# Performance work log

Measured on AMD Instinct MI355X. Metric: run time of the kernel, lower is better.

Reference implementation:

```python
import jax, jax.numpy as jnp
import numpy as np

B, L, T, V = 64, 512, 1000, 256
E, H, M, S = 256, 512, 80, 128  # text_embed, hidden, n_mels, speaker_dim


def lstm_scan(x, Wih, Whh, b):
    # x: [T, B, D]; torch gate order i, f, g, o; bias = b_ih + b_hh fused
    Bn = x.shape[1]
    Hn = Whh.shape[1]
    h0 = jnp.zeros((Bn, Hn), x.dtype)

    def step(carry, xt):
        h, c = carry
        g = xt @ Wih.T + h @ Whh.T + b
        i, f, gg, o = jnp.split(g, 4, axis=-1)
        c = jax.nn.sigmoid(f) * c + jax.nn.sigmoid(i) * jnp.tanh(gg)
        h = jax.nn.sigmoid(o) * jnp.tanh(c)
        return (h, c), h

    _, ys = jax.lax.scan(step, (h0, h0), x)
    return ys  # [T, B, H]


def setup_inputs() -> dict:
    key = jax.random.key(0)
    ks = jax.random.split(key, 32)
    r = lambda i, shp: (jax.random.normal(ks[i], shp, jnp.float32) * 0.1)
    Hd = H // 2  # 256, per-direction biLSTM hidden
    inp = {
        "text_input": jax.random.randint(ks[0], (B, L), 0, V),
        "speaker_embedding": jax.random.normal(ks[1], (B, S), jnp.float32),
        "target_mel": jax.random.normal(ks[2], (B, T, M), jnp.float32),
        "embed": r(3, (V, E)),
        # bidirectional text LSTM (hidden//2 per direction)
        "enc_Wih_f": r(4, (4 * Hd, E)), "enc_Whh_f": r(5, (4 * Hd, Hd)), "enc_b_f": r(6, (4 * Hd,)),
        "enc_Wih_b": r(7, (4 * Hd, E)), "enc_Whh_b": r(8, (4 * Hd, Hd)), "enc_b_b": r(9, (4 * Hd,)),
        # speaker projection MLP
        "sp_W1": r(10, (H, S)), "sp_b1": r(11, (H,)),
        "sp_W2": r(12, (H, H)), "sp_b2": r(13, (H,)),
        # 2-layer decoder LSTM, input = H + M = 592
        "dec_Wih0": r(14, (4 * H, H + M)), "dec_Whh0": r(15, (4 * H, H)), "dec_b0": r(16, (4 * H,)),
        "dec_Wih1": r(17, (4 * H, H)), "dec_Whh1": r(18, (4 * H, H)), "dec_b1": r(19, (4 * H,)),
        # mel projection MLP
        "mel_W1": r(20, (H, H)), "mel_b1": r(21, (H,)),
        "mel_W2": r(22, (M, H)), "mel_b2": r(23, (M,)),
        # stop token projection
        "stop_W": r(24, (1, H)), "stop_b": r(25, (1,)),
    }
    return inp


def reference(text_input, speaker_embedding, target_mel, embed,
              enc_Wih_f, enc_Whh_f, enc_b_f, enc_Wih_b, enc_Whh_b, enc_b_b,
              sp_W1, sp_b1, sp_W2, sp_b2,
              dec_Wih0, dec_Whh0, dec_b0, dec_Wih1, dec_Whh1, dec_b1,
              mel_W1, mel_b1, mel_W2, mel_b2, stop_W, stop_b):
    # --- text encoder: embedding + biLSTM ---
    x = jnp.swapaxes(embed[text_input], 0, 1)  # [L, B, E]
    fwd = lstm_scan(x, enc_Wih_f, enc_Whh_f, enc_b_f)          # [L, B, H/2]
    bwd = lstm_scan(x[::-1], enc_Wih_b, enc_Whh_b, enc_b_b)[::-1]
    text_encoded = jnp.swapaxes(jnp.concatenate([fwd, bwd], -1), 0, 1)  # [B, L, H]

    # --- speaker projection, broadcast over text length ---
    sp = jax.nn.relu(speaker_embedding @ sp_W1.T + sp_b1) @ sp_W2.T + sp_b2  # [B, H]
    encoder_output = text_encoded + sp[:, None, :]  # [B, L, H]

    # --- teacher-forced decoder: query_t = encoder_output[:, t % L] ---
    idx = jnp.arange(T) % L
    query = encoder_output[:, idx]  # [B, T, H]
    dec_mel_in = jnp.concatenate(
        [jnp.zeros((B, 1, M), target_mel.dtype), target_mel[:, :-1]], axis=1)  # [B, T, M]
    rnn_in = jnp.swapaxes(jnp.concatenate([dec_mel_in, query], -1), 0, 1)  # [T, B, H+M]

    h1 = lstm_scan(rnn_in, dec_Wih0, dec_Whh0, dec_b0)  # [T, B, H]
    h2 = lstm_scan(h1, dec_Wih1, dec_Whh1, dec_b1)      # [T, B, H]
    out = jnp.swapaxes(h2, 0, 1)  # [B, T, H]

    mel_outputs = jax.nn.relu(out @ mel_W1.T + mel_b1) @ mel_W2.T + mel_b2  # [B, T, M]
    stop_outputs = out @ stop_W.T + stop_b  # [B, T, 1]
    return mel_outputs, stop_outputs
```

## Files before the change

### kernel.cpp

```cpp
#include <hip/hip_runtime.h>
#include <cstdint>
#include <cstddef>


#define DEVI __device__ __forceinline__

typedef short bf16x8 __attribute__((ext_vector_type(8)));
typedef float f32x4 __attribute__((ext_vector_type(4)));
typedef unsigned short u16x4 __attribute__((ext_vector_type(4)));

constexpr int B_ = 64, L_ = 512, T_ = 1000, E_ = 256, H_ = 512, M_ = 80, S_ = 128, Hd_ = 256;

DEVI unsigned short f2bs(float f) {
  unsigned u = __builtin_bit_cast(unsigned, f);
  unsigned r = u + 0x7fffu + ((u >> 16) & 1u);
  return (unsigned short)(r >> 16);
}
DEVI float b2f(unsigned short s) { return __builtin_bit_cast(float, (unsigned)s << 16); }
DEVI void split2(float v, unsigned short& hi, unsigned short& lo) {
  hi = f2bs(v);
  lo = f2bs(v - b2f(hi));
}

DEVI float sigm(float x) { x = fminf(fmaxf(x, -30.f), 30.f); return 1.f / (1.f + __expf(-x)); }
DEVI float tanh_(float x) { x = fminf(fmaxf(x, -15.f), 15.f); float e = __expf(2.f * x); return (e - 1.f) / (e + 1.f); }

DEVI f32x4 mfma16(bf16x8 a, bf16x8 b, f32x4 c) {
  return __builtin_amdgcn_mfma_f32_16x16x32_bf16(a, b, c, 0, 0, 0);
}

DEVI void ld16c(bf16x8& r, const unsigned short* p) {
  asm volatile("global_load_dwordx4 %0, %1, off sc0 sc1" : "=v"(r) : "v"(p));
}
DEVI void st4c(unsigned short* p, unsigned v) {
  asm volatile("global_store_dword %0, %1, off sc0 sc1" :: "v"(p), "v"(v));
}
DEVI void st8c(unsigned short* p, u16x4 v) {
  asm volatile("global_store_dwordx2 %0, %1, off sc0 sc1" :: "v"(p), "v"(v));
}
#define VM_DRAIN() do { asm volatile("s_waitcnt vmcnt(0)" ::: "memory"); \
                        __builtin_amdgcn_sched_barrier(0); } while (0)
#define VM_WAIT8_OR_0(LAST) do { \
    if (LAST) asm volatile("s_waitcnt vmcnt(0)" ::: "memory"); \
    else      asm volatile("s_waitcnt vmcnt(8)" ::: "memory"); \
    __builtin_amdgcn_sched_barrier(0); } while (0)

struct Bar { int sub[8][64]; int master[64]; int release[64]; };

DEVI void grid_bar(Bar* bb, int nwg, int step) {
  __syncthreads();
  if (threadIdx.x == 0) {
    const int per = nwg >> 3;
    int old = __hip_atomic_fetch_add(&bb->sub[blockIdx.x & 7][0], 1, __ATOMIC_RELAXED, __HIP_MEMORY_SCOPE_AGENT);
    if (old == per * (step + 1) - 1) {
      int om = __hip_atomic_fetch_add(&bb->master[0], 1, __ATOMIC_RELAXED, __HIP_MEMORY_SCOPE_AGENT);
      if (om == 8 * (step + 1) - 1)
        __hip_atomic_fetch_add(&bb->release[0], 1, __ATOMIC_RELAXED, __HIP_MEMORY_SCOPE_AGENT);
    }
    while (__hip_atomic_fetch_add(&bb->release[0], 0, __ATOMIC_RELAXED, __HIP_MEMORY_SCOPE_AGENT) < step + 1)
      __builtin_amdgcn_s_sleep(2);
  }
  __syncthreads();
}

__global__ void k_prep(const float* __restrict__ embed, const float* __restrict__ tmel,
                       const float* __restrict__ mw1, const float* __restrict__ mw2,
                       unsigned short* emb_h, unsigned short* emb_l,
                       unsigned short* mel_h, unsigned short* mel_l,
                       unsigned short* w1_bf, unsigned short* w2_bf) {
  const long long stride = (long long)gridDim.x * blockDim.x;
  const long long i0 = (long long)blockIdx.x * blockDim.x + threadIdx.x;
  for (long long i = i0; i < 256 * 256; i += stride) {
    unsigned short h, l; split2(embed[i], h, l);
    emb_h[i] = h; emb_l[i] = l;
  }
  for (long long i = i0; i < (long long)T_ * B_ * 96; i += stride) {
    int c = (int)(i % 96);
    long long tb = i / 96;
    int b = (int)(tb % B_);
    int t = (int)(tb / B_);
    float v = 0.f;
    if (t > 0 && c < 80) v = tmel[((long long)b * T_ + (t - 1)) * M_ + c];
    unsigned short h, l; split2(v, h, l);
    mel_h[i] = h; mel_l[i] = l;
  }
  for (long long i = i0; i < 512 * 512; i += stride) w1_bf[i] = f2bs(mw1[i]);
  for (long long i = i0; i < 80 * 512; i += stride) w2_bf[i] = f2bs(mw2[i]);
}

__global__ void __launch_bounds__(512) k_sp(const float* __restrict__ spk,
                                            const float* __restrict__ w1, const float* __restrict__ b1,
                                            const float* __restrict__ w2, const float* __restrict__ b2,
                                            float* sp) {
  __shared__ float t1[512];
  const int b = blockIdx.x, j = threadIdx.x;
  float a = b1[j];
  const float* sr = spk + b * S_;
  for (int k = 0; k < S_; ++k) a += sr[k] * w1[j * S_ + k];
  t1[j] = fmaxf(a, 0.f);
  __syncthreads();
  float a2 = b2[j];
  for (int k = 0; k < H_; ++k) a2 += t1[k] * w2[j * H_ + k];
  sp[b * H_ + j] = a2;
}

constexpr int ENC_LDS = 2 * 16 * 4 * 64 * 16 + 4 * 64 * 16 * 4 + 256;

__global__ void __launch_bounds__(256) k_enc(
    const int* __restrict__ text,
    const float* __restrict__ WihF, const float* __restrict__ WhhF, const float* __restrict__ bF,
    const float* __restrict__ WihB, const float* __restrict__ WhhB, const float* __restrict__ bB,
    const unsigned short* __restrict__ emb_h, const unsigned short* __restrict__ emb_l,
    const float* __restrict__ sp,
    unsigned short* hench, unsigned short* hencl,
    unsigned short* ench, unsigned short* encl, Bar* bar) {
  extern __shared__ char lds[];
  unsigned short* Wh = (unsigned short*)lds;
  unsigned short* Wl = Wh + 16 * 4 * 64 * 8;
  float* G = (float*)(lds + 2 * 16 * 4 * 64 * 16);
  float* bias = G + 4 * 64 * 16;

  const int wg = blockIdx.x;
  const int dir = wg >> 4;
  const int jhb = (wg & 15) * 16;
  const int tid = threadIdx.x;
  const int wv = tid >> 6, ln = tid & 63, lg = ln >> 4, lr = ln & 15;

  const float* Wih = dir ? WihB : WihF;
  const float* Whh = dir ? WhhB : WhhF;
  const float* bb = dir ? bB : bF;

  for (int s = tid; s < 16 * 4 * 64; s += 256) {
    int kb = s >> 8, g = (s >> 6) & 3, l = s & 63;
    int R = g * Hd_ + jhb + (l & 15);
    int k0 = kb * 32 + (l >> 4) * 8;
    const float* src = (k0 < E_) ? (Wih + (size_t)R * E_ + k0) : (Whh + (size_t)R * Hd_ + (k0 - E_));
    bf16x8 vh, vl;
#pragma unroll
    for (int j = 0; j < 8; ++j) {
      unsigned short a, b; split2(src[j], a, b);
      vh[j] = (short)a; vl[j] = (short)b;
    }
    *(bf16x8*)(Wh + (size_t)s * 8) = vh;
    *(bf16x8*)(Wl + (size_t)s * 8) = vl;
  }
  if (tid < 64) bias[tid] = bb[(tid >> 4) * Hd_ + jhb + (tid & 15)];

  const int eb = tid >> 2, ej0 = (tid & 3) * 4;
  float c4[4] = {0.f, 0.f, 0.f, 0.f};
  float spv[4];
#pragma unroll
  for (int q = 0; q < 4; ++q) spv[q] = sp[eb * H_ + dir * Hd_ + jhb + ej0 + q];

  __syncthreads();

  for (int t = 0; t < L_; ++t) {
    const int tpos = dir ? (L_ - 1 - t) : t;
    const unsigned short* hsh = hench + (size_t)((t & 1) * 2 + dir) * B_ * Hd_;
    const unsigned short* hsl = hencl + (size_t)((t & 1) * 2 + dir) * B_ * Hd_;
    unsigned short* hdh = hench + (size_t)(((t + 1) & 1) * 2 + dir) * B_ * Hd_;
    unsigned short* hdl = hencl + (size_t)(((t + 1) & 1) * 2 + dir) * B_ * Hd_;

    for (int i = tid; i < 4096; i += 256) G[i] = bias[((i >> 10) << 4) + (i & 15)];

    int tix[4];
#pragma unroll
    for (int m = 0; m < 4; ++m) tix[m] = text[(16 * m + lr) * L_ + tpos];

    f32x4 acc[4][4];
#pragma unroll
    for (int g = 0; g < 4; ++g)
#pragma unroll
      for (int m = 0; m < 4; ++m) acc[g][m] = (f32x4){0.f, 0.f, 0.f, 0.f};

    auto MFE = [&](int kb, bf16x8 (&ah)[4], bf16x8 (&al)[4]) {
#pragma unroll
      for (int g = 0; g < 4; ++g) {
        bf16x8 bh = *(bf16x8*)(Wh + ((size_t)(kb * 4 + g) * 64 + ln) * 8);
        bf16x8 bl = *(bf16x8*)(Wl + ((size_t)(kb * 4 + g) * 64 + ln) * 8);
#pragma unroll
        for (int m = 0; m < 4; ++m) {
          acc[g][m] = mfma16(ah[m], bh, acc[g][m]);
          acc[g][m] = mfma16(al[m], bh, acc[g][m]);
          acc[g][m] = mfma16(ah[m], bl, acc[g][m]);
        }
      }
    };

    for (int kb = wv; kb < 8; kb += 4) {
      int k0 = kb * 32 + lg * 8;
      bf16x8 ah[4], al[4];
#pragma unroll
      for (int m = 0; m < 4; ++m) {
        ah[m] = *(const bf16x8*)(emb_h + (size_t)tix[m] * E_ + k0);
        al[m] = *(const bf16x8*)(emb_l + (size_t)tix[m] * E_ + k0);
      }
      MFE(kb, ah, al);
    }
    {
      auto issueE = [&](int kb, bf16x8 (&ah)[4], bf16x8 (&al)[4]) {
        int k = kb * 32 + lg * 8 - E_;
#pragma unroll
        for (int m = 0; m < 4; ++m) {
          ld16c(ah[m], hsh + (size_t)(16 * m + lr) * Hd_ + k);
          ld16c(al[m], hsl + (size_t)(16 * m + lr) * Hd_ + k);
        }
      };
      bf16x8 A0h[4], A0l[4], A1h[4], A1l[4];
      issueE(8 + wv, A0h, A0l);
      issueE(12 + wv, A1h, A1l);
      VM_WAIT8_OR_0(false);
      MFE(8 + wv, A0h, A0l);
      VM_WAIT8_OR_0(true);
      MFE(12 + wv, A1h, A1l);
    }

    __syncthreads();
#pragma unroll
    for (int g = 0; g < 4; ++g)
#pragma unroll
      for (int m = 0; m < 4; ++m)
#pragma unroll
        for (int r = 0; r < 4; ++r)
          atomicAdd(&G[(g * 64 + 16 * m + 4 * lg + r) * 16 + lr], acc[g][m][r]);
    __syncthreads();

    {
      u16x4 hvh, hvl, ovh, ovl;
#pragma unroll
      for (int q = 0; q < 4; ++q) {
        int jj = ej0 + q;
        float gi = G[(0 * 64 + eb) * 16 + jj];
        float gf = G[(1 * 64 + eb) * 16 + jj];
        float gg = G[(2 * 64 + eb) * 16 + jj];
        float go = G[(3 * 64 + eb) * 16 + jj];
        float cn = sigm(gf) * c4[q] + sigm(gi) * tanh_(gg);
        c4[q] = cn;
        float h = sigm(go) * tanh_(cn);
        unsigned short a, b; split2(h, a, b);
        hvh[q] = a; hvl[q] = b;
        float o = h + spv[q];
        split2(o, a, b);
        ovh[q] = a; ovl[q] = b;
      }
      st8c(hdh + (size_t)eb * Hd_ + jhb + ej0, hvh);
      st8c(hdl + (size_t)eb * Hd_ + jhb + ej0, hvl);
      *(u16x4*)(ench + ((size_t)eb * L_ + tpos) * H_ + dir * Hd_ + jhb + ej0) = ovh;
      *(u16x4*)(encl + ((size_t)eb * L_ + tpos) * H_ + dir * Hd_ + jhb + ej0) = ovl;
    }
    VM_DRAIN();
    grid_bar(bar, 32, t);
  }
}

constexpr int DEC_LDS = 2 * 35 * 2 * 64 * 16 + 4 * 64 * 8 * 4 + 128;

__global__ void __launch_bounds__(256) k_dec(
    const float* __restrict__ Wih0, const float* __restrict__ Whh0, const float* __restrict__ b0,
    const float* __restrict__ Wih1, const float* __restrict__ Whh1, const float* __restrict__ b1,
    const unsigned short* __restrict__ ench, const unsigned short* __restrict__ encl,
    const unsigned short* __restrict__ melh, const unsigned short* __restrict__ mell,
    unsigned short* h0h, unsigned short* h0l,
    unsigned short* h1h, unsigned short* h1l,
    unsigned short* h2_full, Bar* bar) {
  extern __shared__ char lds[];
  const int wg = blockIdx.x;
  const int layer = wg >> 6;
  const int jcb = (wg & 63) * 8;
  const int tid = threadIdx.x, wv = tid >> 6, ln = tid & 63, lg = ln >> 4, lr = ln & 15;
  const int NKB = layer ? 32 : 35;
  unsigned short* Wh = (unsigned short*)lds;
  unsigned short* Wl = Wh + (size_t)NKB * 2 * 64 * 8;
  float* G = (float*)(lds + (size_t)2 * NKB * 2 * 64 * 16);
  float* bias = G + 4 * 64 * 8;

  if (layer == 0) {
    for (int s = tid; s < 35 * 2 * 64; s += 256) {
      int kb = s >> 7, st = (s >> 6) & 1, l = s & 63;
      int n = l & 15;
      int R = (2 * st + (n >> 3)) * H_ + jcb + (n & 7);
      int k0 = kb * 32 + (l >> 4) * 8;
      bf16x8 vh, vl;
      if (k0 < 96) {
#pragma unroll
        for (int j = 0; j < 8; ++j) {
          int c = k0 + j;
          float v = (c < 80) ? Wih0[(size_t)R * 592 + c] : 0.f;
          unsigned short a, b; split2(v, a, b);
          vh[j] = (short)a; vl[j] = (short)b;
        }
      } else if (k0 < 608) {
        const float* src = Wih0 + (size_t)R * 592 + (k0 - 16);
#pragma unroll
        for (int j = 0; j < 8; ++j) {
          unsigned short a, b; split2(src[j], a, b);
          vh[j] = (short)a; vl[j] = (short)b;
        }
      } else {
        const float* src = Whh0 + (size_t)R * H_ + (k0 - 608);
#pragma unroll
        for (int j = 0; j < 8; ++j) {
          unsigned short a, b; split2(src[j], a, b);
          vh[j] = (short)a; vl[j] = (short)b;
        }
      }
      *(bf16x8*)(Wh + (size_t)s * 8) = vh;
      *(bf16x8*)(Wl + (size_t)s * 8) = vl;
    }
    if (tid < 32) bias[tid] = b0[(tid >> 3) * H_ + jcb + (tid & 7)];
  } else {
    for (int s = tid; s < 32 * 2 * 64; s += 256) {
      int kb = s >> 7, st = (s >> 6) & 1, l = s & 63;
      int n = l & 15;
      int R = (2 * st + (n >> 3)) * H_ + jcb + (n & 7);
      int k0 = kb * 32 + (l >> 4) * 8;
      const float* src = (k0 < 512) ? (Wih1 + (size_t)R * H_ + k0) : (Whh1 + (size_t)R * H_ + (k0 - 512));
      bf16x8 vh, vl;
#pragma unroll
      for (int j = 0; j < 8; ++j) {
        unsigned short a, b; split2(src[j], a, b);
        vh[j] = (short)a; vl[j] = (short)b;
      }
      *(bf16x8*)(Wh + (size_t)s * 8) = vh;
      *(bf16x8*)(Wl + (size_t)s * 8) = vl;
    }
    if (tid < 32) bias[tid] = b1[(tid >> 3) * H_ + jcb + (tid & 7)];
  }

  const int ebd = tid & 63, cc0 = (tid >> 6) * 2;
  float c2[2] = {0.f, 0.f};
  __syncthreads();

  for (int tau = 0; tau <= T_; ++tau) {
    const bool active = (layer == 0) ? (tau < T_) : (tau >= 1);
    if (active) {
      const int t = (layer == 0) ? tau : tau - 1;
      for (int i = tid; i < 2048; i += 256) G[i] = bias[((i >> 9) << 3) + (i & 7)];

      f32x4 acc[2][4];
#pragma unroll
      for (int st = 0; st < 2; ++st)
#pragma unroll
        for (int m = 0; m < 4; ++m) acc[st][m] = (f32x4){0.f, 0.f, 0.f, 0.f};

      auto MF = [&](int kb, bf16x8 (&ah)[4], bf16x8 (&al)[4]) {
#pragma unroll
        for (int st = 0; st < 2; ++st) {
          bf16x8 bh = *(bf16x8*)(Wh + ((size_t)(kb * 2 + st) * 64 + ln) * 8);
          bf16x8 bl = *(bf16x8*)(Wl + ((size_t)(kb * 2 + st) * 64 + ln) * 8);
#pragma unroll
          for (int m = 0; m < 4; ++m) {
            acc[st][m] = mfma16(ah[m], bh, acc[st][m]);
            acc[st][m] = mfma16(al[m], bh, acc[st][m]);
            acc[st][m] = mfma16(ah[m], bl, acc[st][m]);
          }
        }
      };

      if (layer == 0) {
        const int tq = t & (L_ - 1);
        const unsigned short* p0h = h0h + (size_t)((tau + 1) & 1) * B_ * H_;
        const unsigned short* p0l = h0l + (size_t)((tau + 1) & 1) * B_ * H_;
        for (int kb = wv; kb < 19; kb += 4) {
          int k0 = kb * 32 + lg * 8;
          bf16x8 ah[4], al[4];
          if (kb < 3) {
#pragma unroll
            for (int m = 0; m < 4; ++m) {
              ah[m] = *(const bf16x8*)(melh + ((size_t)t * B_ + 16 * m + lr) * 96 + k0);
              al[m] = *(const bf16x8*)(mell + ((size_t)t * B_ + 16 * m + lr) * 96 + k0);
            }
          } else {
            int k = k0 - 96;
#pragma unroll
            for (int m = 0; m < 4; ++m) {
              ah[m] = *(const bf16x8*)(ench + ((size_t)(16 * m + lr) * L_ + tq) * H_ + k);
              al[m] = *(const bf16x8*)(encl + ((size_t)(16 * m + lr) * L_ + tq) * H_ + k);
            }
          }
          MF(kb, ah, al);
        }
        {
          auto issue0 = [&](int kb, bf16x8 (&ah)[4], bf16x8 (&al)[4]) {
            int k = kb * 32 + lg * 8 - 608;
#pragma unroll
            for (int m = 0; m < 4; ++m) {
              ld16c(ah[m], p0h + (size_t)(16 * m + lr) * H_ + k);
              ld16c(al[m], p0l + (size_t)(16 * m + lr) * H_ + k);
            }
          };
          const int hkb0 = 19 + ((wv + 1) & 3);
          bf16x8 A0h[4], A0l[4], A1h[4], A1l[4];
          issue0(hkb0, A0h, A0l);
#pragma unroll
          for (int j = 0; j < 4; ++j) {
            const int kb = hkb0 + 4 * j;
            if (j & 1) {
              if (j < 3) issue0(kb + 4, A0h, A0l);
              VM_WAIT8_OR_0(j == 3);
              MF(kb, A1h, A1l);
            } else {
              if (j < 3) issue0(kb + 4, A1h, A1l);
              VM_WAIT8_OR_0(j == 3);
              MF(kb, A0h, A0l);
            }
          }
        }
      } else {
        const unsigned short* q0h = h0h + (size_t)((tau + 1) & 1) * B_ * H_;
        const unsigned short* q0l = h0l + (size_t)((tau + 1) & 1) * B_ * H_;
        const unsigned short* q1h = h1h + (size_t)(tau & 1) * B_ * H_;
        const unsigned short* q1l = h1l + (size_t)(tau & 1) * B_ * H_;
        auto issue1 = [&](int kb, bf16x8 (&ah)[4], bf16x8 (&al)[4]) {
          const unsigned short* sh = (kb < 16) ? q0h : q1h;
          const unsigned short* sl = (kb < 16) ? q0l : q1l;
          int k = (kb * 32 + lg * 8) & 511;
#pragma unroll
          for (int m = 0; m < 4; ++m) {
            ld16c(ah[m], sh + (size_t)(16 * m + lr) * H_ + k);
            ld16c(al[m], sl + (size_t)(16 * m + lr) * H_ + k);
          }
        };
        bf16x8 A0h[4], A0l[4], A1h[4], A1l[4];
        issue1(wv, A0h, A0l);
#pragma unroll
        for (int i = 0; i < 8; ++i) {
          const int kb = wv + 4 * i;
          if (i & 1) {
            if (i < 7) issue1(kb + 4, A0h, A0l);
            VM_WAIT8_OR_0(i == 7);
            MF(kb, A1h, A1l);
          } else {
            if (i < 7) issue1(kb + 4, A1h, A1l);
            VM_WAIT8_OR_0(i == 7);
            MF(kb, A0h, A0l);
          }
        }
      }
      __syncthreads();
#pragma unroll
      for (int st = 0; st < 2; ++st)
#pragma unroll
        for (int m = 0; m < 4; ++m)
#pragma unroll
          for (int r = 0; r < 4; ++r) {
            int g = 2 * st + (lr >> 3), col = lr & 7;
            atomicAdd(&G[(g * 64 + 16 * m + 4 * lg + r) * 8 + col], acc[st][m][r]);
          }
      __syncthreads();

      {
        unsigned short* dh = layer ? (h1h + (size_t)((tau + 1) & 1) * B_ * H_)
                                   : (h0h + (size_t)(tau & 1) * B_ * H_);
        unsigned short* dl = layer ? (h1l + (size_t)((tau + 1) & 1) * B_ * H_)
                                   : (h0l + (size_t)(tau & 1) * B_ * H_);
        unsigned short hh[2], hl[2];
#pragma unroll
        for (int q = 0; q < 2; ++q) {
          int c = cc0 + q;
          float gi = G[(0 * 64 + ebd) * 8 + c];
          float gf = G[(1 * 64 + ebd) * 8 + c];
          float gg = G[(2 * 64 + ebd) * 8 + c];
          float go = G[(3 * 64 + ebd) * 8 + c];
          float cn = sigm(gf) * c2[q] + sigm(gi) * tanh_(gg);
          c2[q] = cn;
          float h = sigm(go) * tanh_(cn);
          split2(h, hh[q], hl[q]);
        }
        unsigned ph = (unsigned)hh[0] | ((unsigned)hh[1] << 16);
        unsigned pl = (unsigned)hl[0] | ((unsigned)hl[1] << 16);
        st4c(dh + (size_t)ebd * H_ + jcb + cc0, ph);
        st4c(dl + (size_t)ebd * H_ + jcb + cc0, pl);
        if (layer) *(unsigned*)(h2_full + ((size_t)t * B_ + ebd) * H_ + jcb + cc0) = ph;
      }
      VM_DRAIN();
    }
    grid_bar(bar, 128, tau);
  }
}

constexpr int MLP_LDS = 64 * 1024;

__global__ void __launch_bounds__(256) k_mlp(
    const unsigned short* __restrict__ h2_full,
    const unsigned short* __restrict__ w1_bf, const unsigned short* __restrict__ w2_bf,
    const float* __restrict__ mb1, const float* __restrict__ mb2,
    const float* __restrict__ stW, const float* __restrict__ stb, float* out) {
  extern __shared__ char lds[];
  const int t = blockIdx.x;
  const int tid = threadIdx.x, wv = tid >> 6, ln = tid & 63, lg = ln >> 4, lr = ln & 15;
  const unsigned short* A = h2_full + (size_t)t * B_ * H_;

  for (int half = 0; half < 2; ++half) {
    const int nb = wv * 8 + half * 4;
    f32x4 acc[4][4];
#pragma unroll
    for (int nn = 0; nn < 4; ++nn) {
      float bv = mb1[(nb + nn) * 16 + lr];
#pragma unroll
      for (int m = 0; m < 4; ++m) acc[m][nn] = (f32x4){bv, bv, bv, bv};
    }
    for (int kb = 0; kb < 16; ++kb) {
      int k0 = kb * 32 + lg * 8;
      bf16x8 afr[4], bfr[4];
#pragma unroll
      for (int m = 0; m < 4; ++m) afr[m] = *(const bf16x8*)(A + (size_t)(16 * m + lr) * H_ + k0);
#pragma unroll
      for (int nn = 0; nn < 4; ++nn) bfr[nn] = *(const bf16x8*)(w1_bf + (size_t)((nb + nn) * 16 + lr) * H_ + k0);
#pragma unroll
      for (int m = 0; m < 4; ++m)
#pragma unroll
        for (int nn = 0; nn < 4; ++nn) acc[m][nn] = mfma16(afr[m], bfr[nn], acc[m][nn]);
    }
#pragma unroll
    for (int m = 0; m < 4; ++m)
#pragma unroll
      for (int nn = 0; nn < 4; ++nn)
#pragma unroll
        for (int r = 0; r < 4; ++r) {
          int row = 16 * m + 4 * lg + r, col = (nb + nn) * 16 + lr;
          *(unsigned short*)(lds + row * 1024 + ((col * 2) ^ ((row & 7) << 4))) =
              f2bs(fmaxf(acc[m][nn][r], 0.f));
        }
  }
  __syncthreads();

  {
    f32x4 acc2[5];
#pragma unroll
    for (int n = 0; n < 5; ++n) {
      float bv = mb2[n * 16 + lr];
      acc2[n] = (f32x4){bv, bv, bv, bv};
    }
    for (int kb = 0; kb < 16; ++kb) {
      int k0 = kb * 32 + lg * 8;
      int row = 16 * wv + lr;
      bf16x8 afr = *(bf16x8*)(lds + row * 1024 + ((k0 * 2) ^ ((row & 7) << 4)));
#pragma unroll
      for (int n = 0; n < 5; ++n) {
        bf16x8 bfr = *(const bf16x8*)(w2_bf + (size_t)(n * 16 + lr) * H_ + k0);
        acc2[n] = mfma16(afr, bfr, acc2[n]);
      }
    }
#pragma unroll
    for (int n = 0; n < 5; ++n)
#pragma unroll
      for (int r = 0; r < 4; ++r) {
        int b = 16 * wv + 4 * lg + r;
        out[((size_t)b * T_ + t) * M_ + n * 16 + lr] = acc2[n][r];
      }
  }

  if (tid < 64) {
    int b = tid;
    float s = stb[0];
    const unsigned short* hp = A + (size_t)b * H_;
    for (int k = 0; k < H_; ++k) s += b2f(hp[k]) * stW[k];
    out[(size_t)B_ * T_ * M_ + (size_t)b * T_ + t] = s;
  }
}

extern "C" void kernel_launch(void* const* d_in, const int* in_sizes, int n_in,
                              void* d_out, int out_size, void* d_ws, size_t ws_size,
                              hipStream_t stream) {
  (void)in_sizes; (void)n_in; (void)out_size; (void)ws_size;
  const int* text = (const int*)d_in[0];
  const float* spk = (const float*)d_in[1];
  const float* tmel = (const float*)d_in[2];
  const float* embed = (const float*)d_in[3];
  const float* eWihF = (const float*)d_in[4];
  const float* eWhhF = (const float*)d_in[5];
  const float* ebF = (const float*)d_in[6];
  const float* eWihB = (const float*)d_in[7];
  const float* eWhhB = (const float*)d_in[8];
  const float* ebB = (const float*)d_in[9];
  const float* spW1 = (const float*)d_in[10];
  const float* spb1 = (const float*)d_in[11];
  const float* spW2 = (const float*)d_in[12];
  const float* spb2 = (const float*)d_in[13];
  const float* dWih0 = (const float*)d_in[14];
  const float* dWhh0 = (const float*)d_in[15];
  const float* db0 = (const float*)d_in[16];
  const float* dWih1 = (const float*)d_in[17];
  const float* dWhh1 = (const float*)d_in[18];
  const float* db1 = (const float*)d_in[19];
  const float* mW1 = (const float*)d_in[20];
  const float* mb1 = (const float*)d_in[21];
  const float* mW2 = (const float*)d_in[22];
  const float* mb2 = (const float*)d_in[23];
  const float* stW = (const float*)d_in[24];
  const float* stb = (const float*)d_in[25];
  float* out = (float*)d_out;

  char* base = (char*)d_ws;
  size_t off = 0;
  auto carve = [&](size_t bytes) -> void* {
    void* p = base + off;
    off += (bytes + 255) & ~(size_t)255;
    return p;
  };
  Bar* barE = (Bar*)carve(sizeof(Bar));
  Bar* barD = (Bar*)carve(sizeof(Bar));
  unsigned short* hench = (unsigned short*)carve((size_t)2 * 2 * B_ * Hd_ * 2);
  unsigned short* hencl = (unsigned short*)carve((size_t)2 * 2 * B_ * Hd_ * 2);
  unsigned short* h0h = (unsigned short*)carve((size_t)2 * B_ * H_ * 2);
  unsigned short* h0l = (unsigned short*)carve((size_t)2 * B_ * H_ * 2);
  unsigned short* h1h = (unsigned short*)carve((size_t)2 * B_ * H_ * 2);
  unsigned short* h1l = (unsigned short*)carve((size_t)2 * B_ * H_ * 2);
  const size_t state_bytes = off;
  float* sp = (float*)carve((size_t)B_ * H_ * 4);
  unsigned short* emb_h = (unsigned short*)carve((size_t)256 * 256 * 2);
  unsigned short* emb_l = (unsigned short*)carve((size_t)256 * 256 * 2);
  unsigned short* mel_h = (unsigned short*)carve((size_t)T_ * B_ * 96 * 2);
  unsigned short* mel_l = (unsigned short*)carve((size_t)T_ * B_ * 96 * 2);
  unsigned short* w1_bf = (unsigned short*)carve((size_t)512 * 512 * 2);
  unsigned short* w2_bf = (unsigned short*)carve((size_t)80 * 512 * 2);
  unsigned short* ench = (unsigned short*)carve((size_t)B_ * L_ * H_ * 2);
  unsigned short* encl = (unsigned short*)carve((size_t)B_ * L_ * H_ * 2);
  unsigned short* h2_full = (unsigned short*)carve((size_t)T_ * B_ * H_ * 2);

  hipMemsetAsync(d_ws, 0, state_bytes, stream);

  hipFuncSetAttribute((const void*)k_enc, hipFuncAttributeMaxDynamicSharedMemorySize, ENC_LDS);
  hipFuncSetAttribute((const void*)k_dec, hipFuncAttributeMaxDynamicSharedMemorySize, DEC_LDS);
  hipFuncSetAttribute((const void*)k_mlp, hipFuncAttributeMaxDynamicSharedMemorySize, MLP_LDS);

  k_prep<<<2048, 256, 0, stream>>>(embed, tmel, mW1, mW2, emb_h, emb_l, mel_h, mel_l, w1_bf, w2_bf);
  k_sp<<<64, 512, 0, stream>>>(spk, spW1, spb1, spW2, spb2, sp);
  k_enc<<<32, 256, ENC_LDS, stream>>>(text, eWihF, eWhhF, ebF, eWihB, eWhhB, ebB,
                                      emb_h, emb_l, sp, hench, hencl, ench, encl, barE);
  k_dec<<<128, 256, DEC_LDS, stream>>>(dWih0, dWhh0, db0, dWih1, dWhh1, db1,
                                       ench, encl, mel_h, mel_l, h0h, h0l, h1h, h1l, h2_full, barD);
  k_mlp<<<1000, 256, MLP_LDS, stream>>>(h2_full, w1_bf, w2_bf, mb1, mb2, stW, stb, out);
}
```

Measured before the change: 38.41 ms.

## Store recurrent hidden state in MFMA fragment layout and poll barrier with plain loads

The encoder and decoder hidden-state exchange buffers now use a fragment-ordered layout that matches the MFMA A-operand, so each lane loads its 16-byte fragment contiguously (lane-linear addresses) instead of row-strided gathers. Writers compute a matching scattered offset when storing. The grid barrier spin now uses a cache-bypassing plain load instead of an atomic add-zero, with a shorter sleep. This targets the latency of the per-step global h reload and barrier release detection, at the cost of scattered small stores and more polling traffic.

```diff
diff --git a/kernel.cpp b/kernel.cpp
--- a/kernel.cpp
+++ b/kernel.cpp
@@ -21,7 +21,6 @@
   hi = f2bs(v);
   lo = f2bs(v - b2f(hi));
 }
-
 DEVI float sigm(float x) { x = fminf(fmaxf(x, -30.f), 30.f); return 1.f / (1.f + __expf(-x)); }
 DEVI float tanh_(float x) { x = fminf(fmaxf(x, -15.f), 15.f); float e = __expf(2.f * x); return (e - 1.f) / (e + 1.f); }
 
@@ -29,7 +28,7 @@
   return __builtin_amdgcn_mfma_f32_16x16x32_bf16(a, b, c, 0, 0, 0);
 }
 
-DEVI void ld16c(bf16x8& r, const unsigned short* p) {
+DEVI void ldc16(bf16x8& r, const unsigned short* p) {
   asm volatile("global_load_dwordx4 %0, %1, off sc0 sc1" : "=v"(r) : "v"(p));
 }
 DEVI void st4c(unsigned short* p, unsigned v) {
@@ -37,6 +36,12 @@
 }
 DEVI void st8c(unsigned short* p, u16x4 v) {
   asm volatile("global_store_dwordx2 %0, %1, off sc0 sc1" :: "v"(p), "v"(v));
+}
+DEVI int pollld(const int* p) {
+  int v;
+  asm volatile("global_load_dword %0, %1, off sc0 sc1\ns_waitcnt vmcnt(0)"
+               : "=v"(v) : "v"(p) : "memory");
+  return v;
 }
 #define VM_DRAIN() do { asm volatile("s_waitcnt vmcnt(0)" ::: "memory"); \
                         __builtin_amdgcn_sched_barrier(0); } while (0)
@@ -51,14 +56,16 @@
   __syncthreads();
   if (threadIdx.x == 0) {
     const int per = nwg >> 3;
-    int old = __hip_atomic_fetch_add(&bb->sub[blockIdx.x & 7][0], 1, __ATOMIC_RELAXED, __HIP_MEMORY_SCOPE_AGENT);
+    int old = __hip_atomic_fetch_add(&bb->sub[blockIdx.x & 7][0], 1,
+                                     __ATOMIC_RELAXED, __HIP_MEMORY_SCOPE_AGENT);
     if (old == per * (step + 1) - 1) {
-      int om = __hip_atomic_fetch_add(&bb->master[0], 1, __ATOMIC_RELAXED, __HIP_MEMORY_SCOPE_AGENT);
+      int om = __hip_atomic_fetch_add(&bb->master[0], 1,
+                                      __ATOMIC_RELAXED, __HIP_MEMORY_SCOPE_AGENT);
       if (om == 8 * (step + 1) - 1)
-        __hip_atomic_fetch_add(&bb->release[0], 1, __ATOMIC_RELAXED, __HIP_MEMORY_SCOPE_AGENT);
-    }
-    while (__hip_atomic_fetch_add(&bb->release[0], 0, __ATOMIC_RELAXED, __HIP_MEMORY_SCOPE_AGENT) < step + 1)
-      __builtin_amdgcn_s_sleep(2);
+        __hip_atomic_fetch_add(&bb->release[0], 1,
+                               __ATOMIC_RELAXED, __HIP_MEMORY_SCOPE_AGENT);
+    }
+    while (pollld(&bb->release[0]) < step + 1) __builtin_amdgcn_s_sleep(1);
   }
   __syncthreads();
 }
@@ -112,7 +119,7 @@
     const float* __restrict__ WihB, const float* __restrict__ WhhB, const float* __restrict__ bB,
     const unsigned short* __restrict__ emb_h, const unsigned short* __restrict__ emb_l,
     const float* __restrict__ sp,
-    unsigned short* hench, unsigned short* hencl,
+    unsigned short* hencfh, unsigned short* hencfl,
     unsigned short* ench, unsigned short* encl, Bar* bar) {
   extern __shared__ char lds[];
   unsigned short* Wh = (unsigned short*)lds;
@@ -152,14 +159,18 @@
 #pragma unroll
   for (int q = 0; q < 4; ++q) spv[q] = sp[eb * H_ + dir * Hd_ + jhb + ej0 + q];
 
+  const int jh = jhb + ej0;
+  const size_t fro = ((size_t)((jh >> 5) * 4 + (eb >> 4)) * 64 +
+                      (((jh >> 3) & 3) * 16 + (eb & 15))) * 8 + (jh & 7);
+
   __syncthreads();
 
   for (int t = 0; t < L_; ++t) {
     const int tpos = dir ? (L_ - 1 - t) : t;
-    const unsigned short* hsh = hench + (size_t)((t & 1) * 2 + dir) * B_ * Hd_;
-    const unsigned short* hsl = hencl + (size_t)((t & 1) * 2 + dir) * B_ * Hd_;
-    unsigned short* hdh = hench + (size_t)(((t + 1) & 1) * 2 + dir) * B_ * Hd_;
-    unsigned short* hdl = hencl + (size_t)(((t + 1) & 1) * 2 + dir) * B_ * Hd_;
+    const unsigned short* hsh = hencfh + ((size_t)((t & 1) * 2 + dir)) * 16384;
+    const unsigned short* hsl = hencfl + ((size_t)((t & 1) * 2 + dir)) * 16384;
+    unsigned short* hdh = hencfh + ((size_t)(((t + 1) & 1) * 2 + dir)) * 16384;
+    unsigned short* hdl = hencfl + ((size_t)(((t + 1) & 1) * 2 + dir)) * 16384;
 
     for (int i = tid; i < 4096; i += 256) G[i] = bias[((i >> 10) << 4) + (i & 15)];
 
@@ -199,12 +210,10 @@
     }
     {
       auto issueE = [&](int kb, bf16x8 (&ah)[4], bf16x8 (&al)[4]) {
-        int k = kb * 32 + lg * 8 - E_;
-#pragma unroll
-        for (int m = 0; m < 4; ++m) {
-          ld16c(ah[m], hsh + (size_t)(16 * m + lr) * Hd_ + k);
-          ld16c(al[m], hsl + (size_t)(16 * m + lr) * Hd_ + k);
-        }
+        const unsigned short* ph = hsh + ((size_t)((kb - 8) * 4) * 64 + ln) * 8;
+        const unsigned short* pl = hsl + ((size_t)((kb - 8) * 4) * 64 + ln) * 8;
+#pragma unroll
+        for (int m = 0; m < 4; ++m) { ldc16(ah[m], ph + m * 512); ldc16(al[m], pl + m * 512); }
       };
       bf16x8 A0h[4], A0l[4], A1h[4], A1l[4];
       issueE(8 + wv, A0h, A0l);
@@ -243,8 +252,8 @@
         split2(o, a, b);
         ovh[q] = a; ovl[q] = b;
       }
-      st8c(hdh + (size_t)eb * Hd_ + jhb + ej0, hvh);
-      st8c(hdl + (size_t)eb * Hd_ + jhb + ej0, hvl);
+      st8c(hdh + fro, hvh);
+      st8c(hdl + fro, hvl);
       *(u16x4*)(ench + ((size_t)eb * L_ + tpos) * H_ + dir * Hd_ + jhb + ej0) = ovh;
       *(u16x4*)(encl + ((size_t)eb * L_ + tpos) * H_ + dir * Hd_ + jhb + ej0) = ovl;
     }
@@ -260,8 +269,8 @@
     const float* __restrict__ Wih1, const float* __restrict__ Whh1, const float* __restrict__ b1,
     const unsigned short* __restrict__ ench, const unsigned short* __restrict__ encl,
     const unsigned short* __restrict__ melh, const unsigned short* __restrict__ mell,
-    unsigned short* h0h, unsigned short* h0l,
-    unsigned short* h1h, unsigned short* h1l,
+    unsigned short* h0fh, unsigned short* h0fl,
+    unsigned short* h1fh, unsigned short* h1fl,
     unsigned short* h2_full, Bar* bar) {
   extern __shared__ char lds[];
   const int wg = blockIdx.x;
@@ -329,6 +338,9 @@
 
   const int ebd = tid & 63, cc0 = (tid >> 6) * 2;
   float c2[2] = {0.f, 0.f};
+  const int j0w = jcb + cc0;
+  const size_t frw = ((size_t)((j0w >> 5) * 4 + (ebd >> 4)) * 64 +
+                      (((j0w >> 3) & 3) * 16 + (ebd & 15))) * 8 + (j0w & 7);
   __syncthreads();
 
   for (int tau = 0; tau <= T_; ++tau) {
@@ -359,8 +371,8 @@
 
       if (layer == 0) {
         const int tq = t & (L_ - 1);
-        const unsigned short* p0h = h0h + (size_t)((tau + 1) & 1) * B_ * H_;
-        const unsigned short* p0l = h0l + (size_t)((tau + 1) & 1) * B_ * H_;
+        const unsigned short* p0h = h0fh + (size_t)((tau + 1) & 1) * 32768;
+        const unsigned short* p0l = h0fl + (size_t)((tau + 1) & 1) * 32768;
         for (int kb = wv; kb < 19; kb += 4) {
           int k0 = kb * 32 + lg * 8;
           bf16x8 ah[4], al[4];
@@ -382,12 +394,10 @@
         }
         {
           auto issue0 = [&](int kb, bf16x8 (&ah)[4], bf16x8 (&al)[4]) {
-            int k = kb * 32 + lg * 8 - 608;
-#pragma unroll
-            for (int m = 0; m < 4; ++m) {
-              ld16c(ah[m], p0h + (size_t)(16 * m + lr) * H_ + k);
-              ld16c(al[m], p0l + (size_t)(16 * m + lr) * H_ + k);
-            }
+            const unsigned short* ph = p0h + ((size_t)((kb - 19) * 4) * 64 + ln) * 8;
+            const unsigned short* pl = p0l + ((size_t)((kb - 19) * 4) * 64 + ln) * 8;
+#pragma unroll
+            for (int m = 0; m < 4; ++m) { ldc16(ah[m], ph + m * 512); ldc16(al[m], pl + m * 512); }
           };
           const int hkb0 = 19 + ((wv + 1) & 3);
           bf16x8 A0h[4], A0l[4], A1h[4], A1l[4];
@@ -407,19 +417,17 @@
           }
         }
       } else {
-        const unsigned short* q0h = h0h + (size_t)((tau + 1) & 1) * B_ * H_;
-        const unsigned short* q0l = h0l + (size_t)((tau + 1) & 1) * B_ * H_;
-        const unsigned short* q1h = h1h + (size_t)(tau & 1) * B_ * H_;
-        const unsigned short* q1l = h1l + (size_t)(tau & 1) * B_ * H_;
+        const unsigned short* q0h = h0fh + (size_t)((tau + 1) & 1) * 32768;
+        const unsigned short* q0l = h0fl + (size_t)((tau + 1) & 1) * 32768;
+        const unsigned short* q1h = h1fh + (size_t)(tau & 1) * 32768;
+        const unsigned short* q1l = h1fl + (size_t)(tau & 1) * 32768;
         auto issue1 = [&](int kb, bf16x8 (&ah)[4], bf16x8 (&al)[4]) {
-          const unsigned short* sh = (kb < 16) ? q0h : q1h;
-          const unsigned short* sl = (kb < 16) ? q0l : q1l;
-          int k = (kb * 32 + lg * 8) & 511;
-#pragma unroll
-          for (int m = 0; m < 4; ++m) {
-            ld16c(ah[m], sh + (size_t)(16 * m + lr) * H_ + k);
-            ld16c(al[m], sl + (size_t)(16 * m + lr) * H_ + k);
-          }
+          const unsigned short* ph = (kb < 16) ? (q0h + ((size_t)(kb * 4) * 64 + ln) * 8)
+                                               : (q1h + ((size_t)((kb - 16) * 4) * 64 + ln) * 8);
+          const unsigned short* pl = (kb < 16) ? (q0l + ((size_t)(kb * 4) * 64 + ln) * 8)
+                                               : (q1l + ((size_t)((kb - 16) * 4) * 64 + ln) * 8);
+#pragma unroll
+          for (int m = 0; m < 4; ++m) { ldc16(ah[m], ph + m * 512); ldc16(al[m], pl + m * 512); }
         };
         bf16x8 A0h[4], A0l[4], A1h[4], A1l[4];
         issue1(wv, A0h, A0l);
@@ -450,10 +458,10 @@
       __syncthreads();
 
       {
-        unsigned short* dh = layer ? (h1h + (size_t)((tau + 1) & 1) * B_ * H_)
-                                   : (h0h + (size_t)(tau & 1) * B_ * H_);
-        unsigned short* dl = layer ? (h1l + (size_t)((tau + 1) & 1) * B_ * H_)
-                                   : (h0l + (size_t)(tau & 1) * B_ * H_);
+        unsigned short* dh = layer ? (h1fh + (size_t)((tau + 1) & 1) * 32768)
+                                   : (h0fh + (size_t)(tau & 1) * 32768);
+        unsigned short* dl = layer ? (h1fl + (size_t)((tau + 1) & 1) * 32768)
+                                   : (h0fl + (size_t)(tau & 1) * 32768);
         unsigned short hh[2], hl[2];
 #pragma unroll
         for (int q = 0; q < 2; ++q) {
@@ -469,8 +477,8 @@
         }
         unsigned ph = (unsigned)hh[0] | ((unsigned)hh[1] << 16);
         unsigned pl = (unsigned)hl[0] | ((unsigned)hl[1] << 16);
-        st4c(dh + (size_t)ebd * H_ + jcb + cc0, ph);
-        st4c(dl + (size_t)ebd * H_ + jcb + cc0, pl);
+        st4c(dh + frw, ph);
+        st4c(dl + frw, pl);
         if (layer) *(unsigned*)(h2_full + ((size_t)t * B_ + ebd) * H_ + jcb + cc0) = ph;
       }
       VM_DRAIN();
@@ -601,12 +609,12 @@
   };
   Bar* barE = (Bar*)carve(sizeof(Bar));
   Bar* barD = (Bar*)carve(sizeof(Bar));
-  unsigned short* hench = (unsigned short*)carve((size_t)2 * 2 * B_ * Hd_ * 2);
-  unsigned short* hencl = (unsigned short*)carve((size_t)2 * 2 * B_ * Hd_ * 2);
-  unsigned short* h0h = (unsigned short*)carve((size_t)2 * B_ * H_ * 2);
-  unsigned short* h0l = (unsigned short*)carve((size_t)2 * B_ * H_ * 2);
-  unsigned short* h1h = (unsigned short*)carve((size_t)2 * B_ * H_ * 2);
-  unsigned short* h1l = (unsigned short*)carve((size_t)2 * B_ * H_ * 2);
+  unsigned short* h0fh = (unsigned short*)carve((size_t)2 * 32768 * 2);
+  unsigned short* h0fl = (unsigned short*)carve((size_t)2 * 32768 * 2);
+  unsigned short* h1fh = (unsigned short*)carve((size_t)2 * 32768 * 2);
+  unsigned short* h1fl = (unsigned short*)carve((size_t)2 * 32768 * 2);
+  unsigned short* hencfh = (unsigned short*)carve((size_t)4 * 16384 * 2);
+  unsigned short* hencfl = (unsigned short*)carve((size_t)4 * 16384 * 2);
   const size_t state_bytes = off;
   float* sp = (float*)carve((size_t)B_ * H_ * 4);
   unsigned short* emb_h = (unsigned short*)carve((size_t)256 * 256 * 2);
@@ -628,8 +636,9 @@
   k_prep<<<2048, 256, 0, stream>>>(embed, tmel, mW1, mW2, emb_h, emb_l, mel_h, mel_l, w1_bf, w2_bf);
   k_sp<<<64, 512, 0, stream>>>(spk, spW1, spb1, spW2, spb2, sp);
   k_enc<<<32, 256, ENC_LDS, stream>>>(text, eWihF, eWhhF, ebF, eWihB, eWhhB, ebB,
-                                      emb_h, emb_l, sp, hench, hencl, ench, encl, barE);
+                                      emb_h, emb_l, sp, hencfh, hencfl, ench, encl, barE);
   k_dec<<<128, 256, DEC_LDS, stream>>>(dWih0, dWhh0, db0, dWih1, dWhh1, db1,
-                                       ench, encl, mel_h, mel_l, h0h, h0l, h1h, h1l, h2_full, barD);
+                                       ench, encl, mel_h, mel_l,
+                                       h0fh, h0fl, h1fh, h1fl, h2_full, barD);
   k_mlp<<<1000, 256, MLP_LDS, stream>>>(h2_full, w1_bf, w2_bf, mb1, mb2, stW, stb, out);
 }
```

Result: faster. 34.66 ms (-9.8%).
